# Optimization experiments

Measured on AMD Instinct MI355X. Metric: run time of the kernel, lower is better.

## Reference

```python
import jax, jax.numpy as jnp
import numpy as np

LN_EPS = 1e-5


def _layer_norm(x, w, b, eps=LN_EPS):
    mu = jnp.mean(x, axis=-1, keepdims=True)
    var = jnp.var(x, axis=-1, keepdims=True)
    return (x - mu) * jax.lax.rsqrt(var + eps) * w + b


def setup_inputs() -> dict:
    key = jax.random.key(0)
    ks = jax.random.split(key, 6)
    H, I, B, S = 1024, 4096, 4, 2048
    return {
        "x": jax.random.normal(ks[0], (B, S, H), jnp.float32),
        "ln_weight": jnp.ones((H,), jnp.float32),
        "ln_bias": jnp.zeros((H,), jnp.float32),
        "i2h_weight": jax.random.normal(ks[1], (2 * I, H), jnp.float32) * 0.02,
        "i2h_bias": jax.random.normal(ks[2], (2 * I,), jnp.float32) * 0.02,
        "h2o_weight": jax.random.normal(ks[3], (H, I), jnp.float32) * 0.02,
        "h2o_bias": jax.random.normal(ks[4], (H,), jnp.float32) * 0.02,
        "post_ln_weight": jnp.ones((H,), jnp.float32),
        "post_ln_bias": jnp.zeros((H,), jnp.float32),
    }


def reference(x, ln_weight, ln_bias, i2h_weight, i2h_bias, h2o_weight, h2o_bias,
              post_ln_weight, post_ln_bias):
    B, S, H = x.shape
    x2 = x.reshape(-1, H)  # [N, H]
    x_ln = _layer_norm(x2, ln_weight, ln_bias)
    # i2h: [N, 2I]
    pre = jnp.einsum('nh,oh->no', x_ln, i2h_weight) + i2h_bias
    I = pre.shape[-1] // 2
    pre_gate, lin = pre[:, :I], pre[:, I:]
    # gated gelu (tanh-approx, matching gelu_fused)
    hid = jax.nn.gelu(pre_gate, approximate=True) * lin
    out = jnp.einsum('ni,oi->no', hid, h2o_weight) + h2o_bias
    out = _layer_norm(out, post_ln_weight, post_ln_bias)
    out = out + x2  # residual (dropout=0)
    return out.reshape(B, S, H)
```

## Files before the change

kernel.cpp:

```cpp
#include <hip/hip_runtime.h>
#include <stdint.h>

#define N_ROWS 8192
#define H_DIM  1024
#define I_DIM  4096

typedef unsigned short u16;
typedef __bf16 bf16x8 __attribute__((ext_vector_type(8)));
typedef float f32x4 __attribute__((ext_vector_type(4)));
typedef u16 u16x4 __attribute__((ext_vector_type(4)));

#define BAR()   asm volatile("s_barrier" ::: "memory")
#define LGKM0() do { asm volatile("s_waitcnt lgkmcnt(0)" ::: "memory"); __builtin_amdgcn_sched_barrier(0); } while (0)
#define VMW(n)  do { asm volatile("s_waitcnt vmcnt(" #n ")" ::: "memory"); __builtin_amdgcn_sched_barrier(0); } while (0)

__device__ __forceinline__ u16 f2bf(float f) {
    union { float f; uint32_t u; } v; v.f = f;
    uint32_t u = v.u;
    u += 0x7FFFu + ((u >> 16) & 1u);
    return (u16)(u >> 16);
}

__device__ __forceinline__ float bf2f(u16 h) {
    union { uint32_t u; float f; } v; v.u = ((uint32_t)h) << 16;
    return v.f;
}

__device__ __forceinline__ float gelu_tanh(float x) {
    float u = 0.7978845608028654f * (x + 0.044715f * x * x * x);
    u = fminf(fmaxf(u, -15.f), 15.f);
    float e = __expf(2.f * u);
    float t = (e - 1.f) / (e + 1.f);
    return 0.5f * x * (1.f + t);
}

__device__ __forceinline__ void load_lds16(const void* g, void* l) {
    auto gp = reinterpret_cast<const __attribute__((address_space(1))) uint32_t*>(
        reinterpret_cast<uintptr_t>(g));
    auto lp = reinterpret_cast<__attribute__((address_space(3))) uint32_t*>(
        static_cast<uint32_t>(reinterpret_cast<uintptr_t>(l)));
    __builtin_amdgcn_global_load_lds(gp, lp, 16, 0, 0);
}

__global__ __launch_bounds__(512, 2) void gemm1_gated(
    const u16* __restrict__ A, const u16* __restrict__ W,
    const float* __restrict__ bias, u16* __restrict__ hid)
{
    __shared__ u16 lds[2 * 32768];
    const int t = threadIdx.x;
    const int lane = t & 63, wid = t >> 6;
    const int wm = wid >> 2, wn = wid & 3;
    const int g = lane >> 4, r16 = lane & 15;

    const int brow = blockIdx.y * 256;
    const int bcol = blockIdx.x * 128;

    const int tr = t >> 2;
    const int swz8 = ((t & 3) ^ ((t >> 3) & 3)) * 8;
    const u16* pA  = A + (size_t)(brow + tr) * H_DIM + swz8;
    const u16* pBg = W + (size_t)(bcol + tr) * H_DIM + swz8;
    const u16* pBl = W + (size_t)(I_DIM + bcol + tr) * H_DIM + swz8;
    const int dst = t * 8;

    const int sl    = (g ^ ((r16 >> 1) & 3)) * 8;
    const int rdA   = (wm * 128 + r16) * 32 + sl;
    const int rdBg  = 16384 + (wn * 32 + r16) * 32 + sl;
    const int rdBl  = rdBg + 4096;

    f32x4 accg[8][2] = {};
    f32x4 accl[8][2] = {};

#pragma unroll
    for (int s = 0; s < 2; ++s) {
        load_lds16(pA + s * 32,                 lds + s * 8192 + dst);
        load_lds16(pA + 128 * H_DIM + s * 32,   lds + s * 8192 + 4096 + dst);
        load_lds16(pBg + s * 32,                lds + 16384 + s * 8192 + dst);
        load_lds16(pBl + s * 32,                lds + 16384 + s * 8192 + 4096 + dst);
    }
    VMW(4); BAR();

    const int NT = H_DIM / 64;
    for (int kt = 0; kt < NT; ++kt) {
        const u16* lA = lds + (kt & 1) * 32768;
        u16* dS = lds + ((kt & 1) ^ 1) * 32768;
        const bool st = (kt + 1 < NT);
        const int k1 = (kt + 1) * 64;
        const bool tail = (kt == NT - 1);

#pragma unroll
        for (int ks = 0; ks < 2; ++ks) {
            bf16x8 af[8], bg[2], bl[2];
#pragma unroll
            for (int m = 0; m < 8; ++m) af[m] = *(const bf16x8*)(lA + ks * 8192 + rdA + m * 512);
#pragma unroll
            for (int n = 0; n < 2; ++n) {
                bg[n] = *(const bf16x8*)(lA + ks * 8192 + rdBg + n * 512);
                bl[n] = *(const bf16x8*)(lA + ks * 8192 + rdBl + n * 512);
            }
            if (st) {
                load_lds16(pA + k1 + ks * 32,               dS + ks * 8192 + dst);
                load_lds16(pA + 128 * H_DIM + k1 + ks * 32, dS + ks * 8192 + 4096 + dst);
                load_lds16(pBg + k1 + ks * 32,              dS + 16384 + ks * 8192 + dst);
                load_lds16(pBl + k1 + ks * 32,              dS + 16384 + ks * 8192 + 4096 + dst);
            }
            if (tail) { VMW(0); } else { VMW(4); }
            BAR(); LGKM0();
            __builtin_amdgcn_s_setprio(1);
#pragma unroll
            for (int m = 0; m < 8; ++m)
#pragma unroll
                for (int n = 0; n < 2; ++n) {
                    accg[m][n] = __builtin_amdgcn_mfma_f32_16x16x32_bf16(af[m], bg[n], accg[m][n], 0, 0, 0);
                    accl[m][n] = __builtin_amdgcn_mfma_f32_16x16x32_bf16(af[m], bl[n], accl[m][n], 0, 0, 0);
                }
            __builtin_amdgcn_s_setprio(0);
            BAR();
        }
    }

#pragma unroll
    for (int n = 0; n < 2; ++n) {
        const int cg = bcol + wn * 32 + n * 16 + r16;
        const float bgv = bias[cg], blv = bias[I_DIM + cg];
#pragma unroll
        for (int m = 0; m < 8; ++m) {
            const int row = brow + wm * 128 + m * 16 + g * 4;
            u16* hp = hid + (size_t)row * I_DIM + cg;
#pragma unroll
            for (int r = 0; r < 4; ++r) {
                float gate = accg[m][n][r] + bgv;
                float lin  = accl[m][n][r] + blv;
                hp[(size_t)r * I_DIM] = f2bf(gelu_tanh(gate) * lin);
            }
        }
    }
}

__global__ __launch_bounds__(512, 2) void gemm2_k(
    const u16* __restrict__ A, const u16* __restrict__ W,
    const float* __restrict__ bias, u16* __restrict__ opb)
{
    __shared__ u16 lds[2 * 24576];
    const int t = threadIdx.x;
    const int lane = t & 63, wid = t >> 6;
    const int wm = wid >> 1, wn = wid & 1;
    const int g = lane >> 4, r16 = lane & 15;

    const int brow = blockIdx.y * 256;
    const int bcol = blockIdx.x * 128;

    const int tr = t >> 2;
    const int swz8 = ((t & 3) ^ ((t >> 3) & 3)) * 8;
    const u16* pA = A + (size_t)(brow + tr) * I_DIM + swz8;
    const u16* pB = W + (size_t)(bcol + tr) * I_DIM + swz8;
    const int dst = t * 8;

    const int sl   = (g ^ ((r16 >> 1) & 3)) * 8;
    const int rdA  = (wm * 64 + r16) * 32 + sl;
    const int rdB  = 16384 + (wn * 64 + r16) * 32 + sl;

    f32x4 acc[4][4] = {};

#pragma unroll
    for (int s = 0; s < 2; ++s) {
        load_lds16(pA + s * 32,               lds + s * 8192 + dst);
        load_lds16(pA + 128 * I_DIM + s * 32, lds + s * 8192 + 4096 + dst);
        load_lds16(pB + s * 32,               lds + 16384 + s * 4096 + dst);
    }
    VMW(3); BAR();

    const int NT = I_DIM / 64;
    for (int kt = 0; kt < NT; ++kt) {
        const u16* lA = lds + (kt & 1) * 24576;
        u16* dS = lds + ((kt & 1) ^ 1) * 24576;
        const bool st = (kt + 1 < NT);
        const int k1 = (kt + 1) * 64;
        const bool tail = (kt == NT - 1);

#pragma unroll
        for (int ks = 0; ks < 2; ++ks) {
            bf16x8 af[4], bf[4];
#pragma unroll
            for (int m = 0; m < 4; ++m) af[m] = *(const bf16x8*)(lA + ks * 8192 + rdA + m * 512);
#pragma unroll
            for (int n = 0; n < 4; ++n) bf[n] = *(const bf16x8*)(lA + ks * 4096 + rdB + n * 512);
            if (st) {
                load_lds16(pA + k1 + ks * 32,               dS + ks * 8192 + dst);
                load_lds16(pA + 128 * I_DIM + k1 + ks * 32, dS + ks * 8192 + 4096 + dst);
                load_lds16(pB + k1 + ks * 32,               dS + 16384 + ks * 4096 + dst);
            }
            if (tail) { VMW(0); } else { VMW(3); }
            BAR(); LGKM0();
            __builtin_amdgcn_s_setprio(1);
#pragma unroll
            for (int m = 0; m < 4; ++m)
#pragma unroll
                for (int n = 0; n < 4; ++n)
                    acc[m][n] = __builtin_amdgcn_mfma_f32_16x16x32_bf16(af[m], bf[n], acc[m][n], 0, 0, 0);
            __builtin_amdgcn_s_setprio(0);
            BAR();
        }
    }

#pragma unroll
    for (int n = 0; n < 4; ++n) {
        const int cg = bcol + wn * 64 + n * 16 + r16;
        const float bv = bias[cg];
#pragma unroll
        for (int m = 0; m < 4; ++m) {
            const int row = brow + wm * 64 + m * 16 + g * 4;
            u16* op = opb + (size_t)row * H_DIM + cg;
#pragma unroll
            for (int r = 0; r < 4; ++r)
                op[(size_t)r * H_DIM] = f2bf(acc[m][n][r] + bv);
        }
    }
}

__device__ __forceinline__ void block_mean_var(float s, float s2, float* red, int t,
                                               float& mu, float& var) {
#pragma unroll
    for (int off = 32; off > 0; off >>= 1) {
        s  += __shfl_down(s, off);
        s2 += __shfl_down(s2, off);
    }
    const int wid = t >> 6;
    if ((t & 63) == 0) { red[wid] = s; red[4 + wid] = s2; }
    __syncthreads();
    if (t == 0) {
        float a = red[0] + red[1] + red[2] + red[3];
        float b = red[4] + red[5] + red[6] + red[7];
        red[0] = a * (1.f / H_DIM);
        red[1] = b * (1.f / H_DIM);
    }
    __syncthreads();
    mu = red[0];
    var = red[1] - mu * mu;
}

__global__ void ln_pre(const float* __restrict__ x, const float* __restrict__ w,
                       const float* __restrict__ b, u16* __restrict__ xln)
{
    __shared__ float red[8];
    const int row = blockIdx.x, t = threadIdx.x;
    const float4 v = reinterpret_cast<const float4*>(x + (size_t)row * H_DIM)[t];
    float mu, var;
    block_mean_var(v.x + v.y + v.z + v.w,
                   v.x * v.x + v.y * v.y + v.z * v.z + v.w * v.w, red, t, mu, var);
    const float rstd = rsqrtf(var + 1e-5f);
    const float4 wv = reinterpret_cast<const float4*>(w)[t];
    const float4 bv = reinterpret_cast<const float4*>(b)[t];
    u16x4 o;
    o.x = f2bf((v.x - mu) * rstd * wv.x + bv.x);
    o.y = f2bf((v.y - mu) * rstd * wv.y + bv.y);
    o.z = f2bf((v.z - mu) * rstd * wv.z + bv.z);
    o.w = f2bf((v.w - mu) * rstd * wv.w + bv.w);
    reinterpret_cast<u16x4*>(xln + (size_t)row * H_DIM)[t] = o;
}

__global__ void ln_post_res(const u16* __restrict__ op, const float* __restrict__ w,
                            const float* __restrict__ b, const float* __restrict__ x,
                            float* __restrict__ out)
{
    __shared__ float red[8];
    const int row = blockIdx.x, t = threadIdx.x;
    const u16x4 hv = reinterpret_cast<const u16x4*>(op + (size_t)row * H_DIM)[t];
    float4 v;
    v.x = bf2f(hv.x); v.y = bf2f(hv.y); v.z = bf2f(hv.z); v.w = bf2f(hv.w);
    float mu, var;
    block_mean_var(v.x + v.y + v.z + v.w,
                   v.x * v.x + v.y * v.y + v.z * v.z + v.w * v.w, red, t, mu, var);
    const float rstd = rsqrtf(var + 1e-5f);
    const float4 wv = reinterpret_cast<const float4*>(w)[t];
    const float4 bv = reinterpret_cast<const float4*>(b)[t];
    const float4 xv = reinterpret_cast<const float4*>(x + (size_t)row * H_DIM)[t];
    float4 o;
    o.x = (v.x - mu) * rstd * wv.x + bv.x + xv.x;
    o.y = (v.y - mu) * rstd * wv.y + bv.y + xv.y;
    o.z = (v.z - mu) * rstd * wv.z + bv.z + xv.z;
    o.w = (v.w - mu) * rstd * wv.w + bv.w + xv.w;
    reinterpret_cast<float4*>(out + (size_t)row * H_DIM)[t] = o;
}

__global__ void cvt_bf16(const float* __restrict__ in, u16* __restrict__ out, int n4) {
    int i = blockIdx.x * blockDim.x + threadIdx.x;
    if (i >= n4) return;
    float4 v = reinterpret_cast<const float4*>(in)[i];
    u16x4 o = { f2bf(v.x), f2bf(v.y), f2bf(v.z), f2bf(v.w) };
    reinterpret_cast<u16x4*>(out)[i] = o;
}

extern "C" void kernel_launch(void* const* d_in, const int* in_sizes, int n_in,
                              void* d_out, int out_size, void* d_ws, size_t ws_size,
                              hipStream_t stream)
{
    const float* x   = (const float*)d_in[0];
    const float* lnw = (const float*)d_in[1];
    const float* lnb = (const float*)d_in[2];
    const float* w1  = (const float*)d_in[3];
    const float* b1  = (const float*)d_in[4];
    const float* w2  = (const float*)d_in[5];
    const float* b2  = (const float*)d_in[6];
    const float* pw  = (const float*)d_in[7];
    const float* pb  = (const float*)d_in[8];
    float* out = (float*)d_out;

    char* ws = (char*)d_ws;
    u16* xln = (u16*)(ws);
    u16* w1b = (u16*)(ws + (16u << 20));
    u16* hid = (u16*)(ws + (32u << 20));
    u16* w2b = (u16*)(ws);
    u16* opb = (u16*)(ws + (8u << 20));

    cvt_bf16<<<(2 * I_DIM * H_DIM / 4 + 255) / 256, 256, 0, stream>>>(w1, w1b, 2 * I_DIM * H_DIM / 4);
    ln_pre<<<N_ROWS, 256, 0, stream>>>(x, lnw, lnb, xln);
    gemm1_gated<<<dim3(I_DIM / 128, N_ROWS / 256), 512, 0, stream>>>(xln, w1b, b1, hid);
    cvt_bf16<<<(H_DIM * I_DIM / 4 + 255) / 256, 256, 0, stream>>>(w2, w2b, H_DIM * I_DIM / 4);
    gemm2_k<<<dim3(H_DIM / 128, N_ROWS / 256), 512, 0, stream>>>(hid, w2b, b2, opb);
    ln_post_res<<<N_ROWS, 256, 0, stream>>>(opb, pw, pb, x, out);
}
```

Before: 276.9 us.

## Shrink GEMM tiles, use triple-buffered K=32 pipeline, fuse prep kernels

Both GEMMs move to 128-row tiles with a K step of 32 and a three-stage LDS ring. The next-next tile is prefetched before the fragment reads, so there is one barrier per step instead of two per 64-wide step. Occupancy hints rise: gemm1 goes to 4 blocks per CU, and gemm2 drops to 256 threads at 3 blocks per CU. The pre-LayerNorm and both weight bf16 conversions are merged into a single prep launch, with w2b moved to its own workspace region. Smaller tiles mean less data reuse per block and more global traffic, and the removed lgkmcnt waits and sched_barriers leave LDS-read ordering to the compiler.

```diff
diff --git a/kernel.cpp b/kernel.cpp
--- a/kernel.cpp
+++ b/kernel.cpp
@@ -11,8 +11,7 @@
 typedef u16 u16x4 __attribute__((ext_vector_type(4)));
 
 #define BAR()   asm volatile("s_barrier" ::: "memory")
-#define LGKM0() do { asm volatile("s_waitcnt lgkmcnt(0)" ::: "memory"); __builtin_amdgcn_sched_barrier(0); } while (0)
-#define VMW(n)  do { asm volatile("s_waitcnt vmcnt(" #n ")" ::: "memory"); __builtin_amdgcn_sched_barrier(0); } while (0)
+#define VMW(n)  asm volatile("s_waitcnt vmcnt(" #n ")" ::: "memory")
 
 __device__ __forceinline__ u16 f2bf(float f) {
     union { float f; uint32_t u; } v; v.f = f;
@@ -42,89 +41,81 @@
     __builtin_amdgcn_global_load_lds(gp, lp, 16, 0, 0);
 }
 
-__global__ __launch_bounds__(512, 2) void gemm1_gated(
+__global__ __launch_bounds__(512, 4) void gemm1_gated(
     const u16* __restrict__ A, const u16* __restrict__ W,
     const float* __restrict__ bias, u16* __restrict__ hid)
 {
-    __shared__ u16 lds[2 * 32768];
+    __shared__ u16 lds[3 * 12288];
     const int t = threadIdx.x;
     const int lane = t & 63, wid = t >> 6;
     const int wm = wid >> 2, wn = wid & 3;
     const int g = lane >> 4, r16 = lane & 15;
 
-    const int brow = blockIdx.y * 256;
+    const int brow = blockIdx.y * 128;
     const int bcol = blockIdx.x * 128;
 
     const int tr = t >> 2;
-    const int swz8 = ((t & 3) ^ ((t >> 3) & 3)) * 8;
+    const int swz8 = ((t & 3) ^ ((tr >> 1) & 3)) * 8;
     const u16* pA  = A + (size_t)(brow + tr) * H_DIM + swz8;
     const u16* pBg = W + (size_t)(bcol + tr) * H_DIM + swz8;
     const u16* pBl = W + (size_t)(I_DIM + bcol + tr) * H_DIM + swz8;
     const int dst = t * 8;
 
-    const int sl    = (g ^ ((r16 >> 1) & 3)) * 8;
-    const int rdA   = (wm * 128 + r16) * 32 + sl;
-    const int rdBg  = 16384 + (wn * 32 + r16) * 32 + sl;
-    const int rdBl  = rdBg + 4096;
-
-    f32x4 accg[8][2] = {};
-    f32x4 accl[8][2] = {};
-
-#pragma unroll
-    for (int s = 0; s < 2; ++s) {
-        load_lds16(pA + s * 32,                 lds + s * 8192 + dst);
-        load_lds16(pA + 128 * H_DIM + s * 32,   lds + s * 8192 + 4096 + dst);
-        load_lds16(pBg + s * 32,                lds + 16384 + s * 8192 + dst);
-        load_lds16(pBl + s * 32,                lds + 16384 + s * 8192 + 4096 + dst);
-    }
-    VMW(4); BAR();
-
-    const int NT = H_DIM / 64;
+    const int sl  = (g ^ ((r16 >> 1) & 3)) * 8;
+    const int rdA = (wm * 64 + r16) * 32 + sl;
+    const int rdB = 4096 + (wn * 32 + r16) * 32 + sl;
+
+    f32x4 accg[4][2] = {};
+    f32x4 accl[4][2] = {};
+
+#define STG1(S, k0) do { \
+    load_lds16(pA  + (k0), (S) + dst); \
+    load_lds16(pBg + (k0), (S) + 4096 + dst); \
+    load_lds16(pBl + (k0), (S) + 8192 + dst); } while (0)
+
+    STG1(lds, 0);
+    STG1(lds + 12288, 32);
+    VMW(3); BAR();
+
+    const int NT = H_DIM / 32;
+    int bc = 0;
+#pragma unroll 1
     for (int kt = 0; kt < NT; ++kt) {
-        const u16* lA = lds + (kt & 1) * 32768;
-        u16* dS = lds + ((kt & 1) ^ 1) * 32768;
-        const bool st = (kt + 1 < NT);
-        const int k1 = (kt + 1) * 64;
-        const bool tail = (kt == NT - 1);
-
-#pragma unroll
-        for (int ks = 0; ks < 2; ++ks) {
-            bf16x8 af[8], bg[2], bl[2];
-#pragma unroll
-            for (int m = 0; m < 8; ++m) af[m] = *(const bf16x8*)(lA + ks * 8192 + rdA + m * 512);
+        const u16* L = lds + bc * 12288;
+        if (kt + 2 < NT) {
+            u16* S = lds + ((bc + 2 >= 3) ? (bc - 1) : (bc + 2)) * 12288;
+            STG1(S, (kt + 2) * 32);
+        }
+        bf16x8 af[4], bg[2], bl[2];
+#pragma unroll
+        for (int m = 0; m < 4; ++m) af[m] = *(const bf16x8*)(L + rdA + m * 512);
+#pragma unroll
+        for (int n = 0; n < 2; ++n) {
+            bg[n] = *(const bf16x8*)(L + rdB + n * 512);
+            bl[n] = *(const bf16x8*)(L + rdB + 4096 + n * 512);
+        }
+        __builtin_amdgcn_s_setprio(1);
+#pragma unroll
+        for (int m = 0; m < 4; ++m)
 #pragma unroll
             for (int n = 0; n < 2; ++n) {
-                bg[n] = *(const bf16x8*)(lA + ks * 8192 + rdBg + n * 512);
-                bl[n] = *(const bf16x8*)(lA + ks * 8192 + rdBl + n * 512);
+                accg[m][n] = __builtin_amdgcn_mfma_f32_16x16x32_bf16(af[m], bg[n], accg[m][n], 0, 0, 0);
+                accl[m][n] = __builtin_amdgcn_mfma_f32_16x16x32_bf16(af[m], bl[n], accl[m][n], 0, 0, 0);
             }
-            if (st) {
-                load_lds16(pA + k1 + ks * 32,               dS + ks * 8192 + dst);
-                load_lds16(pA + 128 * H_DIM + k1 + ks * 32, dS + ks * 8192 + 4096 + dst);
-                load_lds16(pBg + k1 + ks * 32,              dS + 16384 + ks * 8192 + dst);
-                load_lds16(pBl + k1 + ks * 32,              dS + 16384 + ks * 8192 + 4096 + dst);
-            }
-            if (tail) { VMW(0); } else { VMW(4); }
-            BAR(); LGKM0();
-            __builtin_amdgcn_s_setprio(1);
-#pragma unroll
-            for (int m = 0; m < 8; ++m)
-#pragma unroll
-                for (int n = 0; n < 2; ++n) {
-                    accg[m][n] = __builtin_amdgcn_mfma_f32_16x16x32_bf16(af[m], bg[n], accg[m][n], 0, 0, 0);
-                    accl[m][n] = __builtin_amdgcn_mfma_f32_16x16x32_bf16(af[m], bl[n], accl[m][n], 0, 0, 0);
-                }
-            __builtin_amdgcn_s_setprio(0);
-            BAR();
-        }
-    }
+        __builtin_amdgcn_s_setprio(0);
+        if (kt + 2 < NT) { VMW(3); } else { VMW(0); }
+        BAR();
+        bc = (bc == 2) ? 0 : bc + 1;
+    }
+#undef STG1
 
 #pragma unroll
     for (int n = 0; n < 2; ++n) {
         const int cg = bcol + wn * 32 + n * 16 + r16;
         const float bgv = bias[cg], blv = bias[I_DIM + cg];
 #pragma unroll
-        for (int m = 0; m < 8; ++m) {
-            const int row = brow + wm * 128 + m * 16 + g * 4;
+        for (int m = 0; m < 4; ++m) {
+            const int row = brow + wm * 64 + m * 16 + g * 4;
             u16* hp = hid + (size_t)row * I_DIM + cg;
 #pragma unroll
             for (int r = 0; r < 4; ++r) {
@@ -136,71 +127,67 @@
     }
 }
 
-__global__ __launch_bounds__(512, 2) void gemm2_k(
+__global__ __launch_bounds__(256, 3) void gemm2_k(
     const u16* __restrict__ A, const u16* __restrict__ W,
     const float* __restrict__ bias, u16* __restrict__ opb)
 {
-    __shared__ u16 lds[2 * 24576];
+    __shared__ u16 lds[3 * 8192];
     const int t = threadIdx.x;
     const int lane = t & 63, wid = t >> 6;
     const int wm = wid >> 1, wn = wid & 1;
     const int g = lane >> 4, r16 = lane & 15;
 
-    const int brow = blockIdx.y * 256;
+    const int brow = blockIdx.y * 128;
     const int bcol = blockIdx.x * 128;
 
     const int tr = t >> 2;
-    const int swz8 = ((t & 3) ^ ((t >> 3) & 3)) * 8;
+    const int swz8 = ((t & 3) ^ ((tr >> 1) & 3)) * 8;
     const u16* pA = A + (size_t)(brow + tr) * I_DIM + swz8;
     const u16* pB = W + (size_t)(bcol + tr) * I_DIM + swz8;
     const int dst = t * 8;
 
-    const int sl   = (g ^ ((r16 >> 1) & 3)) * 8;
-    const int rdA  = (wm * 64 + r16) * 32 + sl;
-    const int rdB  = 16384 + (wn * 64 + r16) * 32 + sl;
+    const int sl  = (g ^ ((r16 >> 1) & 3)) * 8;
+    const int rdA = (wm * 64 + r16) * 32 + sl;
+    const int rdB = 4096 + (wn * 64 + r16) * 32 + sl;
 
     f32x4 acc[4][4] = {};
 
-#pragma unroll
-    for (int s = 0; s < 2; ++s) {
-        load_lds16(pA + s * 32,               lds + s * 8192 + dst);
-        load_lds16(pA + 128 * I_DIM + s * 32, lds + s * 8192 + 4096 + dst);
-        load_lds16(pB + s * 32,               lds + 16384 + s * 4096 + dst);
-    }
-    VMW(3); BAR();
-
-    const int NT = I_DIM / 64;
+#define STG2(S, k0) do { \
+    load_lds16(pA + (k0),                      (S) + dst); \
+    load_lds16(pA + (size_t)64 * I_DIM + (k0), (S) + 2048 + dst); \
+    load_lds16(pB + (k0),                      (S) + 4096 + dst); \
+    load_lds16(pB + (size_t)64 * I_DIM + (k0), (S) + 6144 + dst); } while (0)
+
+    STG2(lds, 0);
+    STG2(lds + 8192, 32);
+    VMW(4); BAR();
+
+    const int NT = I_DIM / 32;
+    int bc = 0;
+#pragma unroll 1
     for (int kt = 0; kt < NT; ++kt) {
-        const u16* lA = lds + (kt & 1) * 24576;
-        u16* dS = lds + ((kt & 1) ^ 1) * 24576;
-        const bool st = (kt + 1 < NT);
-        const int k1 = (kt + 1) * 64;
-        const bool tail = (kt == NT - 1);
-
-#pragma unroll
-        for (int ks = 0; ks < 2; ++ks) {
-            bf16x8 af[4], bf[4];
-#pragma unroll
-            for (int m = 0; m < 4; ++m) af[m] = *(const bf16x8*)(lA + ks * 8192 + rdA + m * 512);
-#pragma unroll
-            for (int n = 0; n < 4; ++n) bf[n] = *(const bf16x8*)(lA + ks * 4096 + rdB + n * 512);
-            if (st) {
-                load_lds16(pA + k1 + ks * 32,               dS + ks * 8192 + dst);
-                load_lds16(pA + 128 * I_DIM + k1 + ks * 32, dS + ks * 8192 + 4096 + dst);
-                load_lds16(pB + k1 + ks * 32,               dS + 16384 + ks * 4096 + dst);
-            }
-            if (tail) { VMW(0); } else { VMW(3); }
-            BAR(); LGKM0();
-            __builtin_amdgcn_s_setprio(1);
-#pragma unroll
-            for (int m = 0; m < 4; ++m)
-#pragma unroll
-                for (int n = 0; n < 4; ++n)
-                    acc[m][n] = __builtin_amdgcn_mfma_f32_16x16x32_bf16(af[m], bf[n], acc[m][n], 0, 0, 0);
-            __builtin_amdgcn_s_setprio(0);
-            BAR();
-        }
-    }
+        const u16* L = lds + bc * 8192;
+        if (kt + 2 < NT) {
+            u16* S = lds + ((bc + 2 >= 3) ? (bc - 1) : (bc + 2)) * 8192;
+            STG2(S, (kt + 2) * 32);
+        }
+        bf16x8 af[4], bf[4];
+#pragma unroll
+        for (int m = 0; m < 4; ++m) af[m] = *(const bf16x8*)(L + rdA + m * 512);
+#pragma unroll
+        for (int n = 0; n < 4; ++n) bf[n] = *(const bf16x8*)(L + rdB + n * 512);
+        __builtin_amdgcn_s_setprio(1);
+#pragma unroll
+        for (int m = 0; m < 4; ++m)
+#pragma unroll
+            for (int n = 0; n < 4; ++n)
+                acc[m][n] = __builtin_amdgcn_mfma_f32_16x16x32_bf16(af[m], bf[n], acc[m][n], 0, 0, 0);
+        __builtin_amdgcn_s_setprio(0);
+        if (kt + 2 < NT) { VMW(4); } else { VMW(0); }
+        BAR();
+        bc = (bc == 2) ? 0 : bc + 1;
+    }
+#undef STG2
 
 #pragma unroll
     for (int n = 0; n < 4; ++n) {
@@ -238,24 +225,39 @@
     var = red[1] - mu * mu;
 }
 
-__global__ void ln_pre(const float* __restrict__ x, const float* __restrict__ w,
-                       const float* __restrict__ b, u16* __restrict__ xln)
+__global__ __launch_bounds__(256) void prep(
+    const float* __restrict__ x, const float* __restrict__ lnw,
+    const float* __restrict__ lnb, u16* __restrict__ xln,
+    const float* __restrict__ w1, u16* __restrict__ w1b,
+    const float* __restrict__ w2, u16* __restrict__ w2b)
 {
     __shared__ float red[8];
-    const int row = blockIdx.x, t = threadIdx.x;
-    const float4 v = reinterpret_cast<const float4*>(x + (size_t)row * H_DIM)[t];
-    float mu, var;
-    block_mean_var(v.x + v.y + v.z + v.w,
-                   v.x * v.x + v.y * v.y + v.z * v.z + v.w * v.w, red, t, mu, var);
-    const float rstd = rsqrtf(var + 1e-5f);
-    const float4 wv = reinterpret_cast<const float4*>(w)[t];
-    const float4 bv = reinterpret_cast<const float4*>(b)[t];
-    u16x4 o;
-    o.x = f2bf((v.x - mu) * rstd * wv.x + bv.x);
-    o.y = f2bf((v.y - mu) * rstd * wv.y + bv.y);
-    o.z = f2bf((v.z - mu) * rstd * wv.z + bv.z);
-    o.w = f2bf((v.w - mu) * rstd * wv.w + bv.w);
-    reinterpret_cast<u16x4*>(xln + (size_t)row * H_DIM)[t] = o;
+    const int bid = blockIdx.x, t = threadIdx.x;
+    if (bid < N_ROWS) {
+        const float4 v = reinterpret_cast<const float4*>(x + (size_t)bid * H_DIM)[t];
+        float mu, var;
+        block_mean_var(v.x + v.y + v.z + v.w,
+                       v.x * v.x + v.y * v.y + v.z * v.z + v.w * v.w, red, t, mu, var);
+        const float rstd = rsqrtf(var + 1e-5f);
+        const float4 wv = reinterpret_cast<const float4*>(lnw)[t];
+        const float4 bv = reinterpret_cast<const float4*>(lnb)[t];
+        u16x4 o;
+        o.x = f2bf((v.x - mu) * rstd * wv.x + bv.x);
+        o.y = f2bf((v.y - mu) * rstd * wv.y + bv.y);
+        o.z = f2bf((v.z - mu) * rstd * wv.z + bv.z);
+        o.w = f2bf((v.w - mu) * rstd * wv.w + bv.w);
+        reinterpret_cast<u16x4*>(xln + (size_t)bid * H_DIM)[t] = o;
+    } else if (bid < N_ROWS + 8192) {
+        const int i = (bid - N_ROWS) * 256 + t;
+        const float4 v = reinterpret_cast<const float4*>(w1)[i];
+        u16x4 o = { f2bf(v.x), f2bf(v.y), f2bf(v.z), f2bf(v.w) };
+        reinterpret_cast<u16x4*>(w1b)[i] = o;
+    } else {
+        const int i = (bid - N_ROWS - 8192) * 256 + t;
+        const float4 v = reinterpret_cast<const float4*>(w2)[i];
+        u16x4 o = { f2bf(v.x), f2bf(v.y), f2bf(v.z), f2bf(v.w) };
+        reinterpret_cast<u16x4*>(w2b)[i] = o;
+    }
 }
 
 __global__ void ln_post_res(const u16* __restrict__ op, const float* __restrict__ w,
@@ -282,14 +284,6 @@
     reinterpret_cast<float4*>(out + (size_t)row * H_DIM)[t] = o;
 }
 
-__global__ void cvt_bf16(const float* __restrict__ in, u16* __restrict__ out, int n4) {
-    int i = blockIdx.x * blockDim.x + threadIdx.x;
-    if (i >= n4) return;
-    float4 v = reinterpret_cast<const float4*>(in)[i];
-    u16x4 o = { f2bf(v.x), f2bf(v.y), f2bf(v.z), f2bf(v.w) };
-    reinterpret_cast<u16x4*>(out)[i] = o;
-}
-
 extern "C" void kernel_launch(void* const* d_in, const int* in_sizes, int n_in,
                               void* d_out, int out_size, void* d_ws, size_t ws_size,
                               hipStream_t stream)
@@ -309,13 +303,11 @@
     u16* xln = (u16*)(ws);
     u16* w1b = (u16*)(ws + (16u << 20));
     u16* hid = (u16*)(ws + (32u << 20));
-    u16* w2b = (u16*)(ws);
-    u16* opb = (u16*)(ws + (8u << 20));
-
-    cvt_bf16<<<(2 * I_DIM * H_DIM / 4 + 255) / 256, 256, 0, stream>>>(w1, w1b, 2 * I_DIM * H_DIM / 4);
-    ln_pre<<<N_ROWS, 256, 0, stream>>>(x, lnw, lnb, xln);
-    gemm1_gated<<<dim3(I_DIM / 128, N_ROWS / 256), 512, 0, stream>>>(xln, w1b, b1, hid);
-    cvt_bf16<<<(H_DIM * I_DIM / 4 + 255) / 256, 256, 0, stream>>>(w2, w2b, H_DIM * I_DIM / 4);
-    gemm2_k<<<dim3(H_DIM / 128, N_ROWS / 256), 512, 0, stream>>>(hid, w2b, b2, opb);
+    u16* w2b = (u16*)(ws + (96u << 20));
+    u16* opb = (u16*)(ws);
+
+    prep<<<20480, 256, 0, stream>>>(x, lnw, lnb, xln, w1, w1b, w2, w2b);
+    gemm1_gated<<<dim3(I_DIM / 128, N_ROWS / 128), 512, 0, stream>>>(xln, w1b, b1, hid);
+    gemm2_k<<<dim3(H_DIM / 128, N_ROWS / 128), 256, 0, stream>>>(hid, w2b, b2, opb);
     ln_post_res<<<N_ROWS, 256, 0, stream>>>(opb, pw, pb, x, out);
 }
```

New measurement: 272.0 us. No clear change (-1.8%).
